# Kernel optimization log

Measured on AMD Instinct MI355X. Metric: run time of the kernel, lower is better.

## Reference

```python
import jax, jax.numpy as jnp
import numpy as np

D_MODEL = 2048
HEADS = 16
INNER = 8192
SEQ = 2048
BATCH = 1  # source code's mask.reshape(B,1,L,L) requires B==1
EPS = 1e-5


def _layer_norm(x, gamma, beta):
    mu = jnp.mean(x, axis=-1, keepdims=True)
    var = jnp.mean(jnp.square(x - mu), axis=-1, keepdims=True)
    return (x - mu) * jax.lax.rsqrt(var + EPS) * gamma + beta


def setup_inputs() -> dict:
    key = jax.random.key(0)
    ks = jax.random.split(key, 14)
    s = 0.02
    return {
        "x": jax.random.normal(ks[0], (BATCH, SEQ, D_MODEL), jnp.float32),
        # weights stored as (in, out)
        "Wqkv": jax.random.normal(ks[1], (D_MODEL, 3 * D_MODEL), jnp.float32) * s,
        "bqkv": jnp.zeros((3 * D_MODEL,), jnp.float32),
        "Wo": jax.random.normal(ks[2], (D_MODEL, D_MODEL), jnp.float32) * s,
        "bo": jnp.zeros((D_MODEL,), jnp.float32),
        "W1": jax.random.normal(ks[3], (D_MODEL, INNER), jnp.float32) * s,
        "b1": jnp.zeros((INNER,), jnp.float32),
        "W2": jax.random.normal(ks[4], (INNER, D_MODEL), jnp.float32) * s,
        "b2": jnp.zeros((D_MODEL,), jnp.float32),
        "g1": jnp.ones((D_MODEL,), jnp.float32),
        "be1": jnp.zeros((D_MODEL,), jnp.float32),
        "g2": jnp.ones((D_MODEL,), jnp.float32),
        "be2": jnp.zeros((D_MODEL,), jnp.float32),
    }


def reference(x, Wqkv, bqkv, Wo, bo, W1, b1, W2, b2, g1, be1, g2, be2):
    B, L, D = x.shape
    H, hd = HEADS, D // HEADS
    qkv = x @ Wqkv + bqkv                       # [B,L,3D]
    q, k, v = jnp.split(qkv, 3, axis=-1)
    q = q.reshape(B, L, H, hd)
    k = k.reshape(B, L, H, hd)
    v = v.reshape(B, L, H, hd)
    # NOTE: faithful to source, scale is 1/sqrt(D) not 1/sqrt(head_dim)
    scores = jnp.einsum("bqhd,bkhd->bhqk", q, k) / jnp.sqrt(jnp.float32(D))
    causal = jnp.tril(jnp.ones((L, L), bool))   # [L,L] broadcast over B,H
    scores = jnp.where(causal, scores, -jnp.inf)
    attn = jax.nn.softmax(scores, axis=-1)      # dropout = identity (eval)
    out = jnp.einsum("bhqk,bkhd->bqhd", attn, v).reshape(B, L, D)
    lin = out @ Wo + bo
    h = _layer_norm(x + lin, g1, be1)
    ff = jax.nn.gelu(h @ W1 + b1, approximate=False) @ W2 + b2
    return _layer_norm(h + ff, g2, be2)
```

## Files before the change

### kernel.cpp

```cpp
#include <hip/hip_runtime.h>
#include <hip/hip_bf16.h>

typedef unsigned short u16;
typedef __attribute__((ext_vector_type(8))) short frag8;
typedef __attribute__((ext_vector_type(4))) float facc4;

#define L_SEQ 2048
#define D_MODEL 2048
#define N_HEADS 16
#define HEAD_D 128
#define N_QKV 6144
#define D_INNER 8192

__device__ __forceinline__ u16 f2b(float f) {
    __hip_bfloat16 h = __float2bfloat16(f);
    return *reinterpret_cast<u16*>(&h);
}

__device__ __forceinline__ float b2f(u16 u) {
    __hip_bfloat16 h = *reinterpret_cast<__hip_bfloat16*>(&u);
    return __bfloat162float(h);
}

__device__ __forceinline__ void gload_lds16(const void* g, void* l) {
    __builtin_amdgcn_global_load_lds(
        (const __attribute__((address_space(1))) unsigned int*)g,
        (__attribute__((address_space(3))) unsigned int*)l, 16, 0, 0);
}

__device__ __forceinline__ float gelu_exact(float x) {
    return 0.5f * x * (1.0f + erff(x * 0.7071067811865475f));
}

__global__ __launch_bounds__(256) void cvt_bf16_kernel(const float* __restrict__ in, u16* __restrict__ out, int n) {
    const int i = (blockIdx.x * 256 + threadIdx.x) * 8;
    if (i >= n) return;
    float4 a = *(const float4*)(in + i);
    float4 b = *(const float4*)(in + i + 4);
    u16 tmp[8];
    tmp[0] = f2b(a.x); tmp[1] = f2b(a.y); tmp[2] = f2b(a.z); tmp[3] = f2b(a.w);
    tmp[4] = f2b(b.x); tmp[5] = f2b(b.y); tmp[6] = f2b(b.z); tmp[7] = f2b(b.w);
    *(uint4*)(out + i) = *(uint4*)tmp;
}

__global__ __launch_bounds__(256) void tr_cvt64(const float* __restrict__ in, u16* __restrict__ out, int R, int C) {
    __shared__ float t[64][68];
    const int bx = blockIdx.x * 64;
    const int by = blockIdx.y * 64;
    const int tid = threadIdx.x;
    {
        const int r = tid >> 2;
        const int c4 = (tid & 3) * 16;
        const float* src = in + (size_t)(by + r) * C + bx + c4;
#pragma unroll
        for (int j = 0; j < 4; ++j)
            *(float4*)&t[r][c4 + 4 * j] = *(const float4*)(src + 4 * j);
    }
    __syncthreads();
    {
        const int cc = tid >> 2;
        const int rr0 = (tid & 3) * 16;
        u16 tmp[16];
#pragma unroll
        for (int j = 0; j < 16; ++j) tmp[j] = f2b(t[rr0 + j][cc]);
        u16* dst = out + (size_t)(bx + cc) * R + by + rr0;
        *(uint4*)(dst) = *(uint4*)&tmp[0];
        *(uint4*)(dst + 8) = *(uint4*)&tmp[8];
    }
}

__global__ __launch_bounds__(256) void gemm_bt(const u16* __restrict__ A, const u16* __restrict__ Bt,
                                               const float* __restrict__ bias, float* __restrict__ Cout,
                                               int M, int N, int K) {
    __shared__ u16 lA[128 * 64];
    __shared__ u16 lB[128 * 64];
    const int tid = threadIdx.x;
    const int lane = tid & 63, wid = tid >> 6;
    const int wr = wid >> 1, wc = wid & 1;
    const int l15 = lane & 15, g4 = lane >> 4;
    const int bm = blockIdx.y, bn = blockIdx.x;

    const int arow = tid >> 3;
    const int acol = (tid & 7) * 8;
    const size_t abase = (size_t)(bm * 128) * K + acol;
    const size_t bbase = (size_t)(bn * 128) * K + acol;

    facc4 acc[4][4] = {};

    for (int k0 = 0; k0 < K; k0 += 64) {
        if (k0) __syncthreads();
#pragma unroll
        for (int i = 0; i < 4; i++) {
            gload_lds16(A + abase + (size_t)(i * 32 + arow) * K + k0, &lA[i * 2048 + tid * 8]);
            gload_lds16(Bt + bbase + (size_t)(i * 32 + arow) * K + k0, &lB[i * 2048 + tid * 8]);
        }
        __syncthreads();
#pragma unroll
        for (int kk = 0; kk < 64; kk += 32) {
            frag8 af[4], bf[4];
#pragma unroll
            for (int m = 0; m < 4; m++)
                af[m] = *(const frag8*)&lA[(wr * 64 + m * 16 + l15) * 64 + kk + g4 * 8];
#pragma unroll
            for (int n = 0; n < 4; n++)
                bf[n] = *(const frag8*)&lB[(wc * 64 + n * 16 + l15) * 64 + kk + g4 * 8];
#pragma unroll
            for (int m = 0; m < 4; m++)
#pragma unroll
                for (int n = 0; n < 4; n++)
                    acc[m][n] = __builtin_amdgcn_mfma_f32_16x16x32_bf16(af[m], bf[n], acc[m][n], 0, 0, 0);
        }
    }

    const int row0 = bm * 128 + wr * 64 + g4 * 4;
    const int col0 = bn * 128 + wc * 64 + l15;
#pragma unroll
    for (int n = 0; n < 4; n++) {
        const int col = col0 + n * 16;
        const float bv = bias[col];
#pragma unroll
        for (int m = 0; m < 4; m++)
#pragma unroll
            for (int r = 0; r < 4; r++)
                Cout[(size_t)(row0 + m * 16 + r) * N + col] = acc[m][n][r] + bv;
    }
}

template <int EPI>
__global__ __launch_bounds__(512, 2) void gemm256(const u16* __restrict__ A, const u16* __restrict__ Bt,
                                                  const float* __restrict__ bias, void* __restrict__ Cout,
                                                  float* __restrict__ q0, float* __restrict__ q1,
                                                  float* __restrict__ q2, float* __restrict__ q3,
                                                  int M, int N, int K, int kseg, int nbm) {
    __shared__ u16 lds[2 * 32768];
    const int tid = threadIdx.x;
    const int lane = tid & 63, wid = tid >> 6;
    const int wm = wid >> 2, wn = wid & 3;
    const int l15 = lane & 15, g4 = lane >> 4;

    const int nwg = gridDim.x;
    const int q8 = nwg >> 3;
    const int wg = (blockIdx.x & 7) * q8 + (blockIdx.x >> 3);
    const int bm = wg % nbm, bn = wg / nbm;
    const int kb = blockIdx.z * kseg;
    const int ksz = (blockIdx.z == (int)gridDim.z - 1) ? (K - kb) : kseg;
    const int nt = ksz >> 6;

    const int rr = tid >> 3;
    const int kk8 = tid & 7;
    const int srcE = (kk8 ^ (rr & 7)) << 3;
    const u16* aS = A + (size_t)(bm * 256 + rr) * K + kb + srcE;
    const u16* bS = Bt + (size_t)(bn * 256 + ((rr >> 5) << 6) + (rr & 31)) * K + kb + srcE;
    const size_t r128 = (size_t)128 * K;
    const size_t r64 = (size_t)64 * K;
    const size_t c32 = (size_t)32 * K;

    auto stA = [&](int tt, int h) {
        u16* d = &lds[((tt & 1) << 15) + (h << 13)];
        const u16* g = aS + (size_t)tt * 64 + (h ? r64 : 0);
        gload_lds16(g, d + tid * 8);
        gload_lds16(g + r128, d + 4096 + tid * 8);
    };
    auto stB = [&](int tt, int h) {
        u16* d = &lds[((tt & 1) << 15) + 16384 + (h << 13)];
        const u16* g = bS + (size_t)tt * 64 + (h ? c32 : 0);
        gload_lds16(g, d + tid * 8);
        gload_lds16(g + r128, d + 4096 + tid * 8);
    };

    const int ch0 = (g4 ^ (l15 & 7)) << 3;
    const int ch1 = ch0 ^ 32;
    const int aRdBase = (wm * 64 + l15) * 64;
    const int bRdBase = (wn * 32 + l15) * 64;

    frag8 a[4][2], b0[2][2], b1[2][2];
    facc4 acc[8][4] = {};

    auto rdA = [&](int bufo, int mh) {
#pragma unroll
        for (int mi = 0; mi < 4; ++mi) {
            const int base = bufo + mh * 8192 + aRdBase + mi * 1024;
            a[mi][0] = *(const frag8*)&lds[base + ch0];
            a[mi][1] = *(const frag8*)&lds[base + ch1];
        }
    };
    auto rdB = [&](int bufo, int nh, frag8(&bb)[2][2]) {
#pragma unroll
        for (int ni = 0; ni < 2; ++ni) {
            const int base = bufo + 16384 + nh * 8192 + bRdBase + ni * 1024;
            bb[ni][0] = *(const frag8*)&lds[base + ch0];
            bb[ni][1] = *(const frag8*)&lds[base + ch1];
        }
    };
    auto quad = [&](int mh, int nh, frag8(&bb)[2][2]) {
        __builtin_amdgcn_s_setprio(1);
#pragma unroll
        for (int kh = 0; kh < 2; ++kh)
#pragma unroll
            for (int mi = 0; mi < 4; ++mi)
#pragma unroll
                for (int ni = 0; ni < 2; ++ni)
                    acc[mh * 4 + mi][nh * 2 + ni] =
                        __builtin_amdgcn_mfma_f32_16x16x32_bf16(a[mi][kh], bb[ni][kh],
                                                                acc[mh * 4 + mi][nh * 2 + ni], 0, 0, 0);
        __builtin_amdgcn_s_setprio(0);
    };

#define SB __builtin_amdgcn_sched_barrier(0)
#define BAR __builtin_amdgcn_s_barrier()

    stA(0, 0); stB(0, 0); stB(0, 1); stA(0, 1);
    asm volatile("s_waitcnt vmcnt(4)" ::: "memory");
    BAR; SB;

    for (int t = 0; t < nt; ++t) {
        const int bufo = (t & 1) << 15;
        const bool so = (t + 1 < nt);
        rdA(bufo, 0);
        rdB(bufo, 0, b0);
        if (so) stA(t + 1, 0);
        SB; BAR; SB;
        quad(0, 0, b0);
        if (so) asm volatile("s_waitcnt vmcnt(4)" ::: "memory");
        else    asm volatile("s_waitcnt vmcnt(2)" ::: "memory");
        BAR; SB;
        rdB(bufo, 1, b1);
        if (so) stB(t + 1, 0);
        SB; BAR; SB;
        quad(0, 1, b1);
        if (so) asm volatile("s_waitcnt vmcnt(4)" ::: "memory");
        else    asm volatile("s_waitcnt vmcnt(0)" ::: "memory");
        BAR; SB;
        rdA(bufo, 1);
        if (so) stB(t + 1, 1);
        SB; BAR; SB;
        quad(1, 0, b0);
        BAR; SB;
        if (so) stA(t + 1, 1);
        SB; BAR; SB;
        quad(1, 1, b1);
        if (so) asm volatile("s_waitcnt vmcnt(4)" ::: "memory");
        BAR; SB;
    }
#undef SB
#undef BAR

    const int row0 = bm * 256 + wm * 128 + g4 * 4;
    const int col0 = bn * 256 + wn * 64 + l15;
    float* fout;
    if (EPI == 3) {
        const int z = blockIdx.z;
        fout = (z == 0) ? q0 : (z == 1) ? q1 : (z == 2) ? q2 : q3;
    } else {
        fout = (float*)Cout;
    }
#pragma unroll
    for (int nf = 0; nf < 4; nf++) {
        const int col = col0 + nf * 16;
        const float bv = (EPI == 3) ? 0.0f : bias[col];
#pragma unroll
        for (int mf = 0; mf < 8; mf++) {
#pragma unroll
            for (int r = 0; r < 4; r++) {
                const int row = row0 + mf * 16 + r;
                float v = acc[mf][nf][r] + bv;
                if (EPI == 2) v = gelu_exact(v);
                if (EPI == 0 || EPI == 3)
                    fout[(size_t)row * N + col] = v;
                else
                    ((u16*)Cout)[(size_t)row * N + col] = f2b(v);
            }
        }
    }
}

__global__ __launch_bounds__(256) void attn_kernel(const u16* __restrict__ qkv, u16* __restrict__ out) {
    __shared__ u16 kT[64 * 128];
    __shared__ u16 vT[128 * 64];
    const int h = blockIdx.y;
    const int qb = (blockIdx.y < 8) ? ((int)gridDim.x - 1 - (int)blockIdx.x) : (int)blockIdx.x;
    const int tid = threadIdx.x;
    const int lane = tid & 63, w = tid >> 6;
    const int l15 = lane & 15, g4 = lane >> 4;
    const int q0 = qb * 64 + w * 16;
    const float scale = 0.022097086912079608f;

    frag8 qf[4];
    {
        const u16* qrow = qkv + (size_t)(q0 + l15) * N_QKV + h * HEAD_D + g4 * 8;
#pragma unroll
        for (int c = 0; c < 4; c++) qf[c] = *(const frag8*)(qrow + c * 32);
    }

    float m_run = -1e30f, l_run = 0.0f;
    facc4 o[8] = {};

    const int src0 = ((g4 & 1) << 5) + l15;
    const int src1 = src0 + 16;
    const bool hi = (g4 & 2) != 0;

    const int nt = qb + 1;
    for (int t = 0; t < nt; ++t) {
        const int kbase = t * 64;
        if (t) __syncthreads();
        const u16* kg_ptr = qkv + (size_t)kbase * N_QKV + D_MODEL + h * HEAD_D;
        const u16* vg_ptr = kg_ptr + D_MODEL;
        uint4 vv[4];
#pragma unroll
        for (int i = 0; i < 4; ++i)
            vv[i] = *(const uint4*)(vg_ptr + (size_t)lane * N_QKV + w * 32 + i * 8);
#pragma unroll
        for (int p = 0; p < 4; ++p) {
            const int c = p * 256 + tid;
            const int row = c >> 4;
            const int colb = (c & 15) << 4;
            const int srcb = colb ^ ((row & 7) << 4);
            gload_lds16(kg_ptr + (size_t)row * N_QKV + (srcb >> 1), &kT[c * 8]);
        }
#pragma unroll
        for (int i = 0; i < 4; ++i) {
            const u16* pv = (const u16*)&vv[i];
#pragma unroll
            for (int e = 0; e < 8; ++e) {
                const int d = w * 32 + i * 8 + e;
                vT[d * 64 + ((((lane >> 3) ^ (d & 7)) << 3) | (lane & 7))] = pv[e];
            }
        }
        __syncthreads();

        const bool last = (t == nt - 1);

        float st[16];
        float mx = -1e30f;
#pragma unroll
        for (int ks = 0; ks < 4; ++ks) {
            const bool active = !last || (ks <= w);
            if (active) {
                facc4 s = {};
                const int kl = ks * 16 + l15;
#pragma unroll
                for (int c = 0; c < 4; ++c) {
                    const int colb = (g4 * 16 + c * 64) ^ ((kl & 7) << 4);
                    frag8 kf = *(const frag8*)&kT[kl * 128 + (colb >> 1)];
                    s = __builtin_amdgcn_mfma_f32_16x16x32_bf16(kf, qf[c], s, 0, 0, 0);
                }
#pragma unroll
                for (int r = 0; r < 4; ++r) {
                    float v = s[r] * scale;
                    if (last) {
                        const int key = kbase + ks * 16 + g4 * 4 + r;
                        if (key > q0 + l15) v = -1e30f;
                    }
                    st[ks * 4 + r] = v;
                    mx = fmaxf(mx, v);
                }
            } else {
#pragma unroll
                for (int r = 0; r < 4; ++r) st[ks * 4 + r] = -1e30f;
            }
        }

        mx = fmaxf(mx, __shfl_xor(mx, 16));
        mx = fmaxf(mx, __shfl_xor(mx, 32));
        const bool skip = __all(mx <= m_run + 8.0f);
        const float m_new = skip ? m_run : fmaxf(m_run, mx);
        const float alpha = __expf(m_run - m_new);
        float ps = 0.0f;
        uint2 pb[4];
#pragma unroll
        for (int ks = 0; ks < 4; ++ks) {
            const float p0 = __expf(st[ks * 4 + 0] - m_new);
            const float p1 = __expf(st[ks * 4 + 1] - m_new);
            const float p2 = __expf(st[ks * 4 + 2] - m_new);
            const float p3 = __expf(st[ks * 4 + 3] - m_new);
            ps += (p0 + p1) + (p2 + p3);
            pb[ks].x = (unsigned)f2b(p0) | ((unsigned)f2b(p1) << 16);
            pb[ks].y = (unsigned)f2b(p2) | ((unsigned)f2b(p3) << 16);
        }
        ps += __shfl_xor(ps, 16);
        ps += __shfl_xor(ps, 32);
        l_run = l_run * alpha + ps;
        m_run = m_new;
        if (!skip) {
#pragma unroll
            for (int c8 = 0; c8 < 8; ++c8)
#pragma unroll
                for (int r = 0; r < 4; ++r) o[c8][r] *= alpha;
        }

#pragma unroll
        for (int kp = 0; kp < 2; ++kp) {
            const bool kp_active = !last || (kp == 0) || (w >= 2);
            if (kp_active) {
                const uint2 a = pb[2 * kp], b = pb[2 * kp + 1];
                const unsigned a0 = __shfl(a.x, src0), a1 = __shfl(a.y, src0);
                const unsigned a2 = __shfl(a.x, src1), a3 = __shfl(a.y, src1);
                const unsigned b0 = __shfl(b.x, src0), b1 = __shfl(b.y, src0);
                const unsigned b2 = __shfl(b.x, src1), b3 = __shfl(b.y, src1);
                union { unsigned u[4]; frag8 f; } pu;
                pu.u[0] = hi ? b0 : a0;
                pu.u[1] = hi ? b1 : a1;
                pu.u[2] = hi ? b2 : a2;
                pu.u[3] = hi ? b3 : a3;
                const frag8 pf = pu.f;
#pragma unroll
                for (int c8 = 0; c8 < 8; ++c8) {
                    const int d = c8 * 16 + l15;
                    const int ch = (((kp * 4 + g4) ^ (l15 & 7)) << 3);
                    frag8 vf = *(const frag8*)&vT[d * 64 + ch];
                    o[c8] = __builtin_amdgcn_mfma_f32_16x16x32_bf16(vf, pf, o[c8], 0, 0, 0);
                }
            }
        }
    }

    const float inv_l = 1.0f / l_run;
    u16* orow = out + (size_t)(q0 + l15) * D_MODEL + h * HEAD_D;
#pragma unroll
    for (int c8 = 0; c8 < 8; ++c8) {
        uint2 st2;
        st2.x = (unsigned)f2b(o[c8][0] * inv_l) | ((unsigned)f2b(o[c8][1] * inv_l) << 16);
        st2.y = (unsigned)f2b(o[c8][2] * inv_l) | ((unsigned)f2b(o[c8][3] * inv_l) << 16);
        *(uint2*)&orow[c8 * 16 + g4 * 4] = st2;
    }
}

__global__ __launch_bounds__(256) void ln_kernel(const float* __restrict__ a, const float* __restrict__ b,
                                                 const float* __restrict__ gamma, const float* __restrict__ beta,
                                                 u16* __restrict__ outb) {
    __shared__ float red[8];
    const int row = blockIdx.x;
    const int tid = threadIdx.x;
    const float* pa = a + (size_t)row * D_MODEL;
    const float* pb = b + (size_t)row * D_MODEL;
    float v[8];
    float s = 0.0f, s2 = 0.0f;
#pragma unroll
    for (int i = 0; i < 8; i++) {
        const int c = tid + i * 256;
        const float x = pa[c] + pb[c];
        v[i] = x;
        s += x;
        s2 += x * x;
    }
#pragma unroll
    for (int off = 32; off; off >>= 1) {
        s += __shfl_xor(s, off);
        s2 += __shfl_xor(s2, off);
    }
    if ((tid & 63) == 0) { red[(tid >> 6) * 2] = s; red[(tid >> 6) * 2 + 1] = s2; }
    __syncthreads();
    s = red[0] + red[2] + red[4] + red[6];
    s2 = red[1] + red[3] + red[5] + red[7];
    const float mean = s * (1.0f / D_MODEL);
    const float var = s2 * (1.0f / D_MODEL) - mean * mean;
    const float rstd = rsqrtf(var + 1e-5f);
#pragma unroll
    for (int i = 0; i < 8; i++) {
        const int c = tid + i * 256;
        outb[(size_t)row * D_MODEL + c] = f2b((v[i] - mean) * rstd * gamma[c] + beta[c]);
    }
}

__global__ __launch_bounds__(256) void ln_part_kernel(const u16* __restrict__ hb,
                                                      const float* __restrict__ p0, const float* __restrict__ p1,
                                                      const float* __restrict__ p2, const float* __restrict__ p3,
                                                      int np, const float* __restrict__ bias,
                                                      const float* __restrict__ gamma, const float* __restrict__ beta,
                                                      float* __restrict__ outf) {
    __shared__ float red[8];
    const int row = blockIdx.x;
    const int tid = threadIdx.x;
    const size_t rb = (size_t)row * D_MODEL;
    float v[8];
    float s = 0.0f, s2 = 0.0f;
#pragma unroll
    for (int i = 0; i < 8; i++) {
        const int c = tid + i * 256;
        float x = b2f(hb[rb + c]) + bias[c] + p0[rb + c] + p1[rb + c];
        if (np > 2) x += p2[rb + c];
        if (np > 3) x += p3[rb + c];
        v[i] = x;
        s += x;
        s2 += x * x;
    }
#pragma unroll
    for (int off = 32; off; off >>= 1) {
        s += __shfl_xor(s, off);
        s2 += __shfl_xor(s2, off);
    }
    if ((tid & 63) == 0) { red[(tid >> 6) * 2] = s; red[(tid >> 6) * 2 + 1] = s2; }
    __syncthreads();
    s = red[0] + red[2] + red[4] + red[6];
    s2 = red[1] + red[3] + red[5] + red[7];
    const float mean = s * (1.0f / D_MODEL);
    const float var = s2 * (1.0f / D_MODEL) - mean * mean;
    const float rstd = rsqrtf(var + 1e-5f);
#pragma unroll
    for (int i = 0; i < 8; i++) {
        const int c = tid + i * 256;
        outf[rb + c] = (v[i] - mean) * rstd * gamma[c] + beta[c];
    }
}

extern "C" void kernel_launch(void* const* d_in, const int* in_sizes, int n_in,
                              void* d_out, int out_size, void* d_ws, size_t ws_size,
                              hipStream_t stream) {
    const float* x    = (const float*)d_in[0];
    const float* Wqkv = (const float*)d_in[1];
    const float* bqkv = (const float*)d_in[2];
    const float* Wo   = (const float*)d_in[3];
    const float* bo   = (const float*)d_in[4];
    const float* W1   = (const float*)d_in[5];
    const float* b1   = (const float*)d_in[6];
    const float* W2   = (const float*)d_in[7];
    const float* b2   = (const float*)d_in[8];
    const float* g1   = (const float*)d_in[9];
    const float* be1  = (const float*)d_in[10];
    const float* g2   = (const float*)d_in[11];
    const float* be2  = (const float*)d_in[12];

    char* ws = (char*)d_ws;
    const size_t MB = 1024 * 1024;
    u16*  xb     = (u16*)(ws + 0);
    u16*  WqkvT  = (u16*)(ws + 8 * MB);
    u16*  qkv    = (u16*)(ws + 32 * MB);
    u16*  attn_o = (u16*)(ws + 56 * MB);
    u16*  WoT    = (u16*)(ws + 8 * MB);
    float* proj  = (float*)(ws + 16 * MB);
    u16*  hb     = (u16*)(ws + 0);
    u16*  W1T    = (u16*)(ws + 8 * MB);
    u16*  f1     = (u16*)(ws + 40 * MB);
    u16*  W2T    = (u16*)(ws + 72 * MB);
    float* part0 = (float*)(ws + 8 * MB);
    float* part1 = (float*)(ws + 24 * MB);
    float* part2 = (float*)(ws + 104 * MB);
    float* part3 = (float*)(ws + 120 * MB);

    const int np = (ws_size >= 136 * MB) ? 4 : 3;
    const int kseg = (np == 4) ? 2048 : 2688;

    cvt_bf16_kernel<<<2048, 256, 0, stream>>>(x, xb, L_SEQ * D_MODEL);
    tr_cvt64<<<dim3(N_QKV / 64, D_MODEL / 64), 256, 0, stream>>>(Wqkv, WqkvT, D_MODEL, N_QKV);
    gemm256<1><<<dim3(192, 1, 1), 512, 0, stream>>>(xb, WqkvT, bqkv, qkv, nullptr, nullptr, nullptr, nullptr,
                                                    L_SEQ, N_QKV, D_MODEL, D_MODEL, 8);
    attn_kernel<<<dim3(L_SEQ / 64, N_HEADS), 256, 0, stream>>>(qkv, attn_o);
    tr_cvt64<<<dim3(D_MODEL / 64, D_MODEL / 64), 256, 0, stream>>>(Wo, WoT, D_MODEL, D_MODEL);
    gemm_bt<<<dim3(D_MODEL / 128, L_SEQ / 128), 256, 0, stream>>>(attn_o, WoT, bo, proj, L_SEQ, D_MODEL, D_MODEL);
    ln_kernel<<<L_SEQ, 256, 0, stream>>>(x, proj, g1, be1, hb);
    tr_cvt64<<<dim3(D_INNER / 64, D_MODEL / 64), 256, 0, stream>>>(W1, W1T, D_MODEL, D_INNER);
    gemm256<2><<<dim3(256, 1, 1), 512, 0, stream>>>(hb, W1T, b1, f1, nullptr, nullptr, nullptr, nullptr,
                                                    L_SEQ, D_INNER, D_MODEL, D_MODEL, 8);
    tr_cvt64<<<dim3(D_MODEL / 64, D_INNER / 64), 256, 0, stream>>>(W2, W2T, D_INNER, D_MODEL);
    gemm256<3><<<dim3(64, 1, np), 512, 0, stream>>>(f1, W2T, nullptr, nullptr, part0, part1, part2, part3,
                                                    L_SEQ, D_MODEL, D_INNER, kseg, 8);
    ln_part_kernel<<<L_SEQ, 256, 0, stream>>>(hb, part0, part1, part2, part3, np, b2, g2, be2, (float*)d_out);
}
```

Baseline: 463.7 us.

## Double-buffer K/V tiles in attention and store split-K partials as bf16

The attention kernel now keeps two LDS buffers for K and V. It prefetches the next tile's K (async to LDS) and V (into registers) while computing on the current tile, which leaves one barrier per iteration. Separately, the split-K partial sums of the W2 GEMM are written in bf16 instead of fp32, and the split is fixed at 4 segments. That halves partial-sum traffic and removes the workspace-size check. Storing partials in bf16 costs accuracy, and the doubled LDS use may lower attention occupancy.

```diff
diff --git a/kernel.cpp b/kernel.cpp
--- a/kernel.cpp
+++ b/kernel.cpp
@@ -129,8 +129,8 @@
 template <int EPI>
 __global__ __launch_bounds__(512, 2) void gemm256(const u16* __restrict__ A, const u16* __restrict__ Bt,
                                                   const float* __restrict__ bias, void* __restrict__ Cout,
-                                                  float* __restrict__ q0, float* __restrict__ q1,
-                                                  float* __restrict__ q2, float* __restrict__ q3,
+                                                  u16* __restrict__ q0, u16* __restrict__ q1,
+                                                  u16* __restrict__ q2, u16* __restrict__ q3,
                                                   int M, int N, int K, int kseg, int nbm) {
     __shared__ u16 lds[2 * 32768];
     const int tid = threadIdx.x;
@@ -247,12 +247,10 @@
 
     const int row0 = bm * 256 + wm * 128 + g4 * 4;
     const int col0 = bn * 256 + wn * 64 + l15;
-    float* fout;
+    u16* pout = nullptr;
     if (EPI == 3) {
         const int z = blockIdx.z;
-        fout = (z == 0) ? q0 : (z == 1) ? q1 : (z == 2) ? q2 : q3;
-    } else {
-        fout = (float*)Cout;
+        pout = (z == 0) ? q0 : (z == 1) ? q1 : (z == 2) ? q2 : q3;
     }
 #pragma unroll
     for (int nf = 0; nf < 4; nf++) {
@@ -265,8 +263,10 @@
                 const int row = row0 + mf * 16 + r;
                 float v = acc[mf][nf][r] + bv;
                 if (EPI == 2) v = gelu_exact(v);
-                if (EPI == 0 || EPI == 3)
-                    fout[(size_t)row * N + col] = v;
+                if (EPI == 0)
+                    ((float*)Cout)[(size_t)row * N + col] = v;
+                else if (EPI == 3)
+                    pout[(size_t)row * N + col] = f2b(v);
                 else
                     ((u16*)Cout)[(size_t)row * N + col] = f2b(v);
             }
@@ -275,8 +275,8 @@
 }
 
 __global__ __launch_bounds__(256) void attn_kernel(const u16* __restrict__ qkv, u16* __restrict__ out) {
-    __shared__ u16 kT[64 * 128];
-    __shared__ u16 vT[128 * 64];
+    __shared__ u16 kT[2][64 * 128];
+    __shared__ u16 vT[2][128 * 64];
     const int h = blockIdx.y;
     const int qb = (blockIdx.y < 8) ? ((int)gridDim.x - 1 - (int)blockIdx.x) : (int)blockIdx.x;
     const int tid = threadIdx.x;
@@ -285,6 +285,7 @@
     const int q0 = qb * 64 + w * 16;
     const float scale = 0.022097086912079608f;
 
+    const int sk_row = tid >> 2;
     frag8 qf[4];
     {
         const u16* qrow = qkv + (size_t)(q0 + l15) * N_QKV + h * HEAD_D + g4 * 8;
@@ -300,36 +301,57 @@
     const bool hi = (g4 & 2) != 0;
 
     const int nt = qb + 1;
-    for (int t = 0; t < nt; ++t) {
-        const int kbase = t * 64;
-        if (t) __syncthreads();
+
+    auto stageK = [&](int kbase, int buf) {
         const u16* kg_ptr = qkv + (size_t)kbase * N_QKV + D_MODEL + h * HEAD_D;
-        const u16* vg_ptr = kg_ptr + D_MODEL;
-        uint4 vv[4];
-#pragma unroll
-        for (int i = 0; i < 4; ++i)
-            vv[i] = *(const uint4*)(vg_ptr + (size_t)lane * N_QKV + w * 32 + i * 8);
 #pragma unroll
         for (int p = 0; p < 4; ++p) {
             const int c = p * 256 + tid;
             const int row = c >> 4;
             const int colb = (c & 15) << 4;
             const int srcb = colb ^ ((row & 7) << 4);
-            gload_lds16(kg_ptr + (size_t)row * N_QKV + (srcb >> 1), &kT[c * 8]);
-        }
+            gload_lds16(kg_ptr + (size_t)row * N_QKV + (srcb >> 1), &kT[buf][c * 8]);
+        }
+    };
+    auto loadV = [&](int kbase, uint4 (&vv)[4]) {
+        const u16* vg_ptr = qkv + (size_t)kbase * N_QKV + 2 * D_MODEL + h * HEAD_D;
+#pragma unroll
+        for (int i = 0; i < 4; ++i)
+            vv[i] = *(const uint4*)(vg_ptr + (size_t)lane * N_QKV + w * 32 + i * 8);
+    };
+    auto writeV = [&](const uint4 (&vv)[4], int buf) {
 #pragma unroll
         for (int i = 0; i < 4; ++i) {
             const u16* pv = (const u16*)&vv[i];
 #pragma unroll
             for (int e = 0; e < 8; ++e) {
                 const int d = w * 32 + i * 8 + e;
-                vT[d * 64 + ((((lane >> 3) ^ (d & 7)) << 3) | (lane & 7))] = pv[e];
+                vT[buf][d * 64 + ((((lane >> 3) ^ (d & 7)) << 3) | (lane & 7))] = pv[e];
             }
         }
-        __syncthreads();
-
+    };
+
+    {
+        uint4 vv[4];
+        stageK(0, 0);
+        loadV(0, vv);
+        writeV(vv, 0);
+    }
+    __syncthreads();
+
+    for (int t = 0; t < nt; ++t) {
+        const int buf = t & 1;
+        const int kbase = t * 64;
         const bool last = (t == nt - 1);
 
+        uint4 vv[4];
+        if (!last) {
+            stageK(kbase + 64, buf ^ 1);
+            loadV(kbase + 64, vv);
+        }
+
+        const u16* kTb = kT[buf];
+        const u16* vTb = vT[buf];
         float st[16];
         float mx = -1e30f;
 #pragma unroll
@@ -341,7 +363,7 @@
 #pragma unroll
                 for (int c = 0; c < 4; ++c) {
                     const int colb = (g4 * 16 + c * 64) ^ ((kl & 7) << 4);
-                    frag8 kf = *(const frag8*)&kT[kl * 128 + (colb >> 1)];
+                    frag8 kf = *(const frag8*)&kTb[kl * 128 + (colb >> 1)];
                     s = __builtin_amdgcn_mfma_f32_16x16x32_bf16(kf, qf[c], s, 0, 0, 0);
                 }
 #pragma unroll
@@ -407,11 +429,14 @@
                 for (int c8 = 0; c8 < 8; ++c8) {
                     const int d = c8 * 16 + l15;
                     const int ch = (((kp * 4 + g4) ^ (l15 & 7)) << 3);
-                    frag8 vf = *(const frag8*)&vT[d * 64 + ch];
+                    frag8 vf = *(const frag8*)&vTb[d * 64 + ch];
                     o[c8] = __builtin_amdgcn_mfma_f32_16x16x32_bf16(vf, pf, o[c8], 0, 0, 0);
                 }
             }
         }
+
+        if (!last) writeV(vv, buf ^ 1);
+        __syncthreads();
     }
 
     const float inv_l = 1.0f / l_run;
@@ -463,9 +488,9 @@
 }
 
 __global__ __launch_bounds__(256) void ln_part_kernel(const u16* __restrict__ hb,
-                                                      const float* __restrict__ p0, const float* __restrict__ p1,
-                                                      const float* __restrict__ p2, const float* __restrict__ p3,
-                                                      int np, const float* __restrict__ bias,
+                                                      const u16* __restrict__ p0, const u16* __restrict__ p1,
+                                                      const u16* __restrict__ p2, const u16* __restrict__ p3,
+                                                      const float* __restrict__ bias,
                                                       const float* __restrict__ gamma, const float* __restrict__ beta,
                                                       float* __restrict__ outf) {
     __shared__ float red[8];
@@ -477,9 +502,8 @@
 #pragma unroll
     for (int i = 0; i < 8; i++) {
         const int c = tid + i * 256;
-        float x = b2f(hb[rb + c]) + bias[c] + p0[rb + c] + p1[rb + c];
-        if (np > 2) x += p2[rb + c];
-        if (np > 3) x += p3[rb + c];
+        float x = b2f(hb[rb + c]) + bias[c] +
+                  b2f(p0[rb + c]) + b2f(p1[rb + c]) + b2f(p2[rb + c]) + b2f(p3[rb + c]);
         v[i] = x;
         s += x;
         s2 += x * x;
@@ -532,13 +556,10 @@
     u16*  W1T    = (u16*)(ws + 8 * MB);
     u16*  f1     = (u16*)(ws + 40 * MB);
     u16*  W2T    = (u16*)(ws + 72 * MB);
-    float* part0 = (float*)(ws + 8 * MB);
-    float* part1 = (float*)(ws + 24 * MB);
-    float* part2 = (float*)(ws + 104 * MB);
-    float* part3 = (float*)(ws + 120 * MB);
-
-    const int np = (ws_size >= 136 * MB) ? 4 : 3;
-    const int kseg = (np == 4) ? 2048 : 2688;
+    u16*  part0  = (u16*)(ws + 8 * MB);
+    u16*  part1  = (u16*)(ws + 16 * MB);
+    u16*  part2  = (u16*)(ws + 24 * MB);
+    u16*  part3  = (u16*)(ws + 32 * MB);
 
     cvt_bf16_kernel<<<2048, 256, 0, stream>>>(x, xb, L_SEQ * D_MODEL);
     tr_cvt64<<<dim3(N_QKV / 64, D_MODEL / 64), 256, 0, stream>>>(Wqkv, WqkvT, D_MODEL, N_QKV);
@@ -552,7 +573,7 @@
     gemm256<2><<<dim3(256, 1, 1), 512, 0, stream>>>(hb, W1T, b1, f1, nullptr, nullptr, nullptr, nullptr,
                                                     L_SEQ, D_INNER, D_MODEL, D_MODEL, 8);
     tr_cvt64<<<dim3(D_MODEL / 64, D_INNER / 64), 256, 0, stream>>>(W2, W2T, D_INNER, D_MODEL);
-    gemm256<3><<<dim3(64, 1, np), 512, 0, stream>>>(f1, W2T, nullptr, nullptr, part0, part1, part2, part3,
-                                                    L_SEQ, D_MODEL, D_INNER, kseg, 8);
-    ln_part_kernel<<<L_SEQ, 256, 0, stream>>>(hb, part0, part1, part2, part3, np, b2, g2, be2, (float*)d_out);
-}
+    gemm256<3><<<dim3(64, 1, 4), 512, 0, stream>>>(f1, W2T, nullptr, nullptr, part0, part1, part2, part3,
+                                                   L_SEQ, D_MODEL, D_INNER, 2048, 8);
+    ln_part_kernel<<<L_SEQ, 256, 0, stream>>>(hb, part0, part1, part2, part3, b2, g2, be2, (float*)d_out);
+}
```

Measured after the change: 466.9 us. About the same (+0.7%).
